# Kernel tuning notes

Measured on AMD Instinct MI355X. Metric: run time of the kernel, lower is better.

Reference implementation:

```python
import jax, jax.numpy as jnp
import numpy as np

B, S, E, H, N = 16384, 256, 128, 128, 34  # batch, state_dim, reduced_lang_dim, mlp hidden, N_task
TEMP = 0.1
EPS = 1e-8  # torch cosine_similarity eps


def setup_inputs() -> dict:
    key = jax.random.key(0)
    ks = jax.random.split(key, 12)
    sc = 0.05
    return {
        "state": jax.random.normal(ks[0], (B, S), dtype=jnp.float32),
        "task_id": jax.random.randint(ks[1], (B,), 0, N),
        "prior": jax.random.normal(ks[2], (B, N), dtype=jnp.float32),
        # stacked weights of the 34 per-task MLPs (Linear(S,H) -> ReLU -> Linear(H,H) -> ReLU -> Linear(H,E))
        "W1": jax.random.normal(ks[3], (N, S, H), dtype=jnp.float32) * sc,
        "b1": jax.random.normal(ks[4], (N, H), dtype=jnp.float32) * sc,
        "W2": jax.random.normal(ks[5], (N, H, H), dtype=jnp.float32) * sc,
        "b2": jax.random.normal(ks[6], (N, H), dtype=jnp.float32) * sc,
        "W3": jax.random.normal(ks[7], (N, H, E), dtype=jnp.float32) * sc,
        "b3": jax.random.normal(ks[8], (N, E), dtype=jnp.float32) * sc,
        "lang_emb": jax.random.normal(ks[9], (N, E), dtype=jnp.float32),
    }


def reference(state, task_id, prior, W1, b1, W2, b2, W3, b3, lang_emb):
    # 34 parallel MLPs as a single batched GEMM stack: [B,S] x [N,S,H] -> [B,N,H]
    h = jax.nn.relu(jnp.einsum('bs,nsh->bnh', state, W1) + b1)
    h = jax.nn.relu(jnp.einsum('bnh,nhk->bnk', h, W2) + b2)
    q = jnp.einsum('bnk,nke->bne', h, W3) + b3            # [B,N,E]
    # normalize (torch.norm division, no eps, then cosine_similarity renormalizes -> unit)
    q = q / jnp.linalg.norm(q, axis=-1, keepdims=True)
    lang = lang_emb[task_id]                              # [B,E]
    lang_n = lang / jnp.maximum(jnp.linalg.norm(lang, axis=-1, keepdims=True), EPS)
    cos_sim = jnp.einsum('bne,be->bn', q, lang_n)         # [B,N]
    log_task_prob = jax.nn.log_softmax(cos_sim / TEMP, axis=-1)
    task_prob_prior = jax.nn.softmax(prior, axis=-1)      # exp(log_softmax(prior))
    latent_vec = jnp.einsum('bne,bn->be', q, task_prob_prior)
    latent_target = jax.lax.stop_gradient(q[jnp.arange(B), task_id])  # detach
    rep_vec = jnp.concatenate([state, latent_vec], axis=-1)           # [B, S+E]
    return rep_vec, log_task_prob, latent_target, latent_vec
```

## Files before the change

kernel.cpp:

```cpp
#include <hip/hip_runtime.h>
#include <hip/hip_bf16.h>
#include <hip/hip_fp16.h>
#include <cstdint>
#include <cstddef>

typedef __bf16 bf16;
typedef __attribute__((ext_vector_type(8))) __bf16 bf16x8;
typedef __attribute__((ext_vector_type(16))) float f32x16;

static_assert(sizeof(bf16x8) == 16, "bf16x8 must be 16B");

#define NTASK 34
#define BTOT 16384
#define WSTRIDE 73728

__device__ __forceinline__ f32x16 mfma32(bf16x8 a, bf16x8 b, f32x16 c) {
  return __builtin_amdgcn_mfma_f32_32x32x16_bf16(a, b, c, 0, 0, 0);
}

__device__ __forceinline__ void gload_lds16(const void* g, void* l) {
  __builtin_amdgcn_global_load_lds((__attribute__((address_space(1))) void*)g,
                                   (__attribute__((address_space(3))) void*)l,
                                   16, 0, 0);
}

__device__ __forceinline__ unsigned pack2(float lo, float hi) {
  union { __bf16 h[2]; unsigned u; } v;
  v.h[0] = (__bf16)lo; v.h[1] = (__bf16)hi;
  return v.u;
}

__device__ __forceinline__ void pl32swap(unsigned &a, unsigned &b) {
  asm volatile("v_permlane32_swap_b32 %0, %1" : "+v"(a), "+v"(b));
}

__global__ void prep_all(const float* __restrict__ W1, const float* __restrict__ W2,
                         const float* __restrict__ W3, const float* __restrict__ b1,
                         const float* __restrict__ b2, const float* __restrict__ b3,
                         const float* __restrict__ state,
                         bf16* __restrict__ wdst, bf16* __restrict__ sdst) {
  int bid = blockIdx.x;
  if (bid < 1190) {
    int idx = bid * 256 + threadIdx.x;
    if (idx >= 304640) return;
    int n = idx / (140 * 64);
    int r = idx - n * (140 * 64);
    int bb = r >> 6, l = r & 63;
    const float *W, *bias; int real, mt, ks, Kt;
    size_t off;
    if (bb < 68)       { W = W1; bias = b1; mt = bb / 17; ks = bb - mt * 17; real = 16; Kt = 256;
                         off = (size_t)bb * 512; }
    else if (bb < 104) { W = W2; bias = b2; int t = bb - 68;  mt = t / 9; ks = t - mt * 9; real = 8; Kt = 128;
                         off = 36864 + (size_t)(bb - 68) * 512; }
    else               { W = W3; bias = b3; int t = bb - 104; mt = t / 9; ks = t - mt * 9; real = 8; Kt = 128;
                         off = 36864 + 18432 + (size_t)(bb - 104) * 512; }
    int col = mt * 32 + (l & 31);
    bf16x8 v;
    if (ks < real) {
      int k0 = ks * 16 + ((l >> 5) << 3);
      const float* s = W + ((size_t)n * Kt + k0) * 128 + col;
#pragma unroll
      for (int j = 0; j < 8; ++j) v[j] = (bf16)s[(size_t)j * 128];
    } else {
#pragma unroll
      for (int j = 0; j < 8; ++j) v[j] = (bf16)0.f;
      if (l < 32) v[0] = (bf16)bias[n * 128 + col];
    }
    *(bf16x8*)(wdst + (size_t)n * WSTRIDE + off + l * 8) = v;
  } else {
    int idx = (bid - 1190) * 256 + threadIdx.x;
    int rb = idx >> 10;
    int r = idx & 1023;
    int ks = r >> 6;
    int l = r & 63;
    int b = rb * 32 + (l & 31);
    int k0 = ks * 16 + ((l >> 5) << 3);
    const float* s = state + (size_t)b * 256 + k0;
    bf16x8 v;
#pragma unroll
    for (int j = 0; j < 8; ++j) v[j] = (bf16)s[j];
    *(bf16x8*)(sdst + (size_t)(rb * 16 + ks) * 512 + l * 8) = v;
  }
}

__global__ void prep_langn(const float* __restrict__ lang, float* __restrict__ out) {
  __shared__ float red[2];
  int n = blockIdx.x;
  int t = threadIdx.x;
  float v = lang[(size_t)n * 128 + t];
  float ss = v * v;
#pragma unroll
  for (int m = 1; m < 64; m <<= 1) ss += __shfl_xor(ss, m);
  if ((t & 63) == 0) red[t >> 6] = ss;
  __syncthreads();
  float s = red[0] + red[1];
  float sc = 1.0f / fmaxf(sqrtf(s), 1e-8f);
  out[(size_t)n * 128 + t] = v * sc;
}

__global__ void prep_pprior(const float* __restrict__ prior, float* __restrict__ ppt) {
  int row = blockIdx.x * 4 + (threadIdx.x >> 6);
  int lane = threadIdx.x & 63;
  float v = (lane < NTASK) ? prior[(size_t)row * NTASK + lane] : -INFINITY;
  float m = v;
#pragma unroll
  for (int mm = 1; mm < 64; mm <<= 1) m = fmaxf(m, __shfl_xor(m, mm));
  float e = (lane < NTASK) ? expf(v - m) : 0.0f;
  float s = e;
#pragma unroll
  for (int mm = 1; mm < 64; mm <<= 1) s += __shfl_xor(s, mm);
  if (lane < NTASK) ppt[(size_t)lane * BTOT + row] = e / s;
}


__global__ void __launch_bounds__(512, 2)
pass1_kernel(const int* __restrict__ task_id, const bf16* __restrict__ wstream,
             const bf16* __restrict__ sf, const float* __restrict__ langn,
             const float* __restrict__ pp_t,
             float* __restrict__ cs_t, __half* __restrict__ lat_part,
             float* __restrict__ out_tgt) {
  __shared__ __align__(16) bf16 shA[36864];
  __shared__ __align__(16) bf16 shB[36864];

  const int tid = threadIdx.x;
  const int l = tid & 63;
  const int w = tid >> 6;
  const int hi = l >> 5;
  const int b = l & 31;
  const int tg = blockIdx.x >> 6;
  const int rg = blockIdx.x & 63;
  const int start = tg * 4 + (tg < 2 ? tg : 2);
  const int cnt = 4 + (tg < 2 ? 1 : 0);
  const int row0 = rg * 256 + w * 32 + b;
  const int rb0 = rg * 8 + w;

  int tidn0 = task_id[row0];

  {
    const bf16* wb0 = wstream + (size_t)start * WSTRIDE;
#pragma unroll
    for (int c = 0; c < 9; ++c)
      gload_lds16(wb0 + c * 4096 + tid * 8, shA + c * 4096 + tid * 8);
  }

  union { unsigned u[4]; bf16x8 v; } cf;
  cf.u[0] = (l < 32) ? 0x3f80u : 0u;
  cf.u[1] = 0u; cf.u[2] = 0u; cf.u[3] = 0u;

  f32x16 z;
#pragma unroll
  for (int i = 0; i < 16; ++i) z[i] = 0.f;
  f32x16 lat[4] = {z, z, z, z};

  const bf16* sb0 = sf + (size_t)rb0 * 8192 + l * 8;

  auto transition = [&](f32x16* acc, bf16x8* f) {
#pragma unroll
    for (int mt = 0; mt < 4; ++mt) {
      unsigned p[8];
#pragma unroll
      for (int q = 0; q < 4; ++q) {
        p[2 * q]     = pack2(fmaxf(acc[mt][4 * q + 0], 0.f), fmaxf(acc[mt][4 * q + 1], 0.f));
        p[2 * q + 1] = pack2(fmaxf(acc[mt][4 * q + 2], 0.f), fmaxf(acc[mt][4 * q + 3], 0.f));
      }
      pl32swap(p[0], p[2]); pl32swap(p[1], p[3]);
      pl32swap(p[4], p[6]); pl32swap(p[5], p[7]);
      union { unsigned u[4]; bf16x8 v; } e, o;
      e.u[0] = p[0]; e.u[1] = p[1]; e.u[2] = p[2]; e.u[3] = p[3];
      o.u[0] = p[4]; o.u[1] = p[5]; o.u[2] = p[6]; o.u[3] = p[7];
      f[2 * mt] = e.v; f[2 * mt + 1] = o.v;
    }
  };

  for (int t = 0; t < cnt; ++t) {
    const int n = start + t;
    const bf16* wbase = wstream + (size_t)n * WSTRIDE;

#pragma unroll
    for (int c = 0; c < 9; ++c)
      gload_lds16(wbase + 36864 + c * 4096 + tid * 8, shB + c * 4096 + tid * 8);

    if (t == 0) {
      asm volatile("s_waitcnt vmcnt(9)" ::: "memory");
      __builtin_amdgcn_s_barrier();
    }

    f32x16 acc[4] = {z, z, z, z};

    bf16x8 s0[4];
#pragma unroll
    for (int i = 0; i < 4; ++i) s0[i] = *(const bf16x8*)(sb0 + i * 512);
#pragma unroll
    for (int ks = 0; ks < 16; ++ks) {
      bf16x8 sv = s0[ks & 3];
      if (ks < 12) s0[ks & 3] = *(const bf16x8*)(sb0 + (ks + 4) * 512);
      __builtin_amdgcn_s_setprio(1);
#pragma unroll
      for (int mt = 0; mt < 4; ++mt) {
        bf16x8 wf = *(const bf16x8*)(shA + ((mt * 17 + ks) << 9) + l * 8);
        acc[mt] = mfma32(wf, sv, acc[mt]);
      }
      __builtin_amdgcn_s_setprio(0);
    }
#pragma unroll
    for (int mt = 0; mt < 4; ++mt) {
      bf16x8 wf = *(const bf16x8*)(shA + ((mt * 17 + 16) << 9) + l * 8);
      acc[mt] = mfma32(wf, cf.v, acc[mt]);
    }

    bf16x8 f2[8];
    transition(acc, f2);

    asm volatile("s_waitcnt vmcnt(0)" ::: "memory");
    __builtin_amdgcn_s_barrier();

    if (t + 1 < cnt) {
      const bf16* wnext = wstream + (size_t)(n + 1) * WSTRIDE;
#pragma unroll
      for (int c = 0; c < 9; ++c)
        gload_lds16(wnext + c * 4096 + tid * 8, shA + c * 4096 + tid * 8);
    }
#pragma unroll
    for (int mt = 0; mt < 4; ++mt) acc[mt] = z;
#pragma unroll
    for (int ks = 0; ks < 8; ++ks) {
      __builtin_amdgcn_s_setprio(1);
#pragma unroll
      for (int mt = 0; mt < 4; ++mt) {
        bf16x8 wf = *(const bf16x8*)(shB + ((mt * 9 + ks) << 9) + l * 8);
        acc[mt] = mfma32(wf, f2[ks], acc[mt]);
      }
      __builtin_amdgcn_s_setprio(0);
    }
#pragma unroll
    for (int mt = 0; mt < 4; ++mt) {
      bf16x8 wf = *(const bf16x8*)(shB + ((mt * 9 + 8) << 9) + l * 8);
      acc[mt] = mfma32(wf, cf.v, acc[mt]);
    }

    bf16x8 f3[8];
    transition(acc, f3);

#pragma unroll
    for (int mt = 0; mt < 4; ++mt) acc[mt] = z;
#pragma unroll
    for (int ks = 0; ks < 8; ++ks) {
      __builtin_amdgcn_s_setprio(1);
#pragma unroll
      for (int mt = 0; mt < 4; ++mt) {
        bf16x8 wf = *(const bf16x8*)(shB + ((36 + mt * 9 + ks) << 9) + l * 8);
        acc[mt] = mfma32(wf, f3[ks], acc[mt]);
      }
      __builtin_amdgcn_s_setprio(0);
    }
#pragma unroll
    for (int mt = 0; mt < 4; ++mt) {
      bf16x8 wf = *(const bf16x8*)(shB + ((36 + mt * 9 + 8) << 9) + l * 8);
      acc[mt] = mfma32(wf, cf.v, acc[mt]);
    }

    float ssq = 0.f, dot = 0.f;
    const float* lgb = langn + (size_t)tidn0 * 128;
#pragma unroll
    for (int mt = 0; mt < 4; ++mt)
#pragma unroll
      for (int q = 0; q < 4; ++q) {
        int c0 = mt * 32 + q * 8 + 4 * hi;
        float4 lg = *(const float4*)(lgb + c0);
        float a0 = acc[mt][4 * q + 0], a1 = acc[mt][4 * q + 1];
        float a2 = acc[mt][4 * q + 2], a3 = acc[mt][4 * q + 3];
        ssq += a0 * a0 + a1 * a1 + a2 * a2 + a3 * a3;
        dot += a0 * lg.x + a1 * lg.y + a2 * lg.z + a3 * lg.w;
      }
    ssq += __shfl_xor(ssq, 32);
    dot += __shfl_xor(dot, 32);
    float inv = rsqrtf(ssq);
    if (l < 32) cs_t[(size_t)row0 * NTASK + n] = dot * inv;
    float pwi = pp_t[(size_t)n * BTOT + row0] * inv;
#pragma unroll
    for (int mt = 0; mt < 4; ++mt) lat[mt] += acc[mt] * pwi;
    if (tidn0 == n) {
#pragma unroll
      for (int mt = 0; mt < 4; ++mt)
#pragma unroll
        for (int q = 0; q < 4; ++q) {
          float4 qv = {acc[mt][4 * q + 0] * inv, acc[mt][4 * q + 1] * inv,
                       acc[mt][4 * q + 2] * inv, acc[mt][4 * q + 3] * inv};
          *(float4*)(out_tgt + (size_t)row0 * 128 + mt * 32 + q * 8 + 4 * hi) = qv;
        }
    }

    asm volatile("s_waitcnt vmcnt(0)" ::: "memory");
    __builtin_amdgcn_s_barrier();
  }

  __half* lp = lat_part + ((size_t)tg * BTOT + row0) * 128;
#pragma unroll
  for (int mt = 0; mt < 4; ++mt)
#pragma unroll
    for (int q = 0; q < 4; ++q) {
      int c0 = mt * 32 + q * 8 + 4 * hi;
      union { __half h[4]; uint2 u; } v;
      v.h[0] = __float2half(lat[mt][4 * q + 0]);
      v.h[1] = __float2half(lat[mt][4 * q + 1]);
      v.h[2] = __float2half(lat[mt][4 * q + 2]);
      v.h[3] = __float2half(lat[mt][4 * q + 3]);
      *(uint2*)(lp + c0) = v.u;
    }
}


__global__ void __launch_bounds__(256)
pass3_kernel(const float* __restrict__ state, const float* __restrict__ cs_t,
             const __half* __restrict__ lat_part,
             float* __restrict__ out_rep, float* __restrict__ out_ltp,
             float* __restrict__ out_lat) {
  int w = threadIdx.x >> 6, l = threadIdx.x & 63;
  size_t row = (size_t)blockIdx.x * 4 + w;

  float c = (l < NTASK) ? cs_t[row * NTASK + l] * 10.0f : -1e30f;
  float cm = c;
#pragma unroll
  for (int mm = 1; mm < 64; mm <<= 1) cm = fmaxf(cm, __shfl_xor(cm, mm));
  float ce = (l < NTASK) ? expf(c - cm) : 0.0f;
  float cs = ce;
#pragma unroll
  for (int mm = 1; mm < 64; mm <<= 1) cs += __shfl_xor(cs, mm);
  if (l < NTASK) out_ltp[row * NTASK + l] = c - cm - logf(cs);

  float2 lv = {0.f, 0.f};
#pragma unroll
  for (int g = 0; g < 8; ++g) {
    __half2 p = *(const __half2*)(lat_part + ((size_t)g * BTOT + row) * 128 + 2 * l);
    lv.x += __low2float(p);
    lv.y += __high2float(p);
  }
  *(float2*)(out_lat + row * 128 + 2 * l) = lv;
  *(float2*)(out_rep + row * 384 + 256 + 2 * l) = lv;

  float4 sv = *(const float4*)(state + row * 256 + l * 4);
  *(float4*)(out_rep + row * 384 + l * 4) = sv;
}


extern "C" void kernel_launch(void* const* d_in, const int* in_sizes, int n_in,
                              void* d_out, int out_size, void* d_ws, size_t ws_size,
                              hipStream_t stream) {
  (void)in_sizes; (void)n_in; (void)out_size; (void)ws_size;
  const float* state = (const float*)d_in[0];
  const int* task_id = (const int*)d_in[1];
  const float* prior = (const float*)d_in[2];
  const float* W1 = (const float*)d_in[3];
  const float* b1 = (const float*)d_in[4];
  const float* W2 = (const float*)d_in[5];
  const float* b2 = (const float*)d_in[6];
  const float* W3 = (const float*)d_in[7];
  const float* b3 = (const float*)d_in[8];
  const float* lang = (const float*)d_in[9];

  char* ws = (char*)d_ws;
  bf16* wstream  = (bf16*)(ws + 0);
  bf16* sf       = (bf16*)(ws + 5013504);
  float* langn   = (float*)(ws + 13402112);
  float* pp_t    = (float*)(ws + 13419520);
  float* cs_t    = (float*)(ws + 15647744);
  __half* lat_part = (__half*)(ws + 17875968);

  float* out = (float*)d_out;
  float* out_rep = out;
  float* out_ltp = out + 6291456;
  float* out_tgt = out + 6848512;
  float* out_lat = out + 8945664;

  prep_all<<<3238, 256, 0, stream>>>(W1, W2, W3, b1, b2, b3, state, wstream, sf);
  prep_langn<<<NTASK, 128, 0, stream>>>(lang, langn);
  prep_pprior<<<4096, 256, 0, stream>>>(prior, pp_t);
  pass1_kernel<<<512, 512, 0, stream>>>(task_id, wstream, sf, langn, pp_t,
                                        cs_t, lat_part, out_tgt);
  pass3_kernel<<<4096, 256, 0, stream>>>(state, cs_t, lat_part,
                                         out_rep, out_ltp, out_lat);
}
```

Baseline: 160.7 us.

## Shrink pass1 blocks to 256 threads with single LDS weight buffer; fuse prior softmax

Pass1 now runs 1024 blocks of 256 threads, each covering 128 rows, and keeps a single 72 KB LDS buffer instead of two. Within each task, the W1 stage, then the W2/W3 stage, are streamed into that buffer in turn, with barriers and partial vmcnt waits so the W3 half can arrive while layer 2 computes. The prior softmax is folded into prep_all as extra blocks, which removes one kernel launch. Less LDS per block may allow more resident blocks, but the weight-load latency is now more exposed because the next load cannot start until compute on the buffer has finished. Each block also handles fewer rows, so weights are fetched from L2 twice as often.

```diff
diff --git a/kernel.cpp b/kernel.cpp
--- a/kernel.cpp
+++ b/kernel.cpp
@@ -37,8 +37,9 @@
 __global__ void prep_all(const float* __restrict__ W1, const float* __restrict__ W2,
                          const float* __restrict__ W3, const float* __restrict__ b1,
                          const float* __restrict__ b2, const float* __restrict__ b3,
-                         const float* __restrict__ state,
-                         bf16* __restrict__ wdst, bf16* __restrict__ sdst) {
+                         const float* __restrict__ state, const float* __restrict__ prior,
+                         bf16* __restrict__ wdst, bf16* __restrict__ sdst,
+                         float* __restrict__ ppt) {
   int bid = blockIdx.x;
   if (bid < 1190) {
     int idx = bid * 256 + threadIdx.x;
@@ -67,7 +68,7 @@
       if (l < 32) v[0] = (bf16)bias[n * 128 + col];
     }
     *(bf16x8*)(wdst + (size_t)n * WSTRIDE + off + l * 8) = v;
-  } else {
+  } else if (bid < 3238) {
     int idx = (bid - 1190) * 256 + threadIdx.x;
     int rb = idx >> 10;
     int r = idx & 1023;
@@ -80,6 +81,18 @@
 #pragma unroll
     for (int j = 0; j < 8; ++j) v[j] = (bf16)s[j];
     *(bf16x8*)(sdst + (size_t)(rb * 16 + ks) * 512 + l * 8) = v;
+  } else {
+    int row = (bid - 3238) * 4 + (threadIdx.x >> 6);
+    int lane = threadIdx.x & 63;
+    float v = (lane < NTASK) ? prior[(size_t)row * NTASK + lane] : -INFINITY;
+    float m = v;
+#pragma unroll
+    for (int mm = 1; mm < 64; mm <<= 1) m = fmaxf(m, __shfl_xor(m, mm));
+    float e = (lane < NTASK) ? expf(v - m) : 0.0f;
+    float s = e;
+#pragma unroll
+    for (int mm = 1; mm < 64; mm <<= 1) s += __shfl_xor(s, mm);
+    if (lane < NTASK) ppt[(size_t)lane * BTOT + row] = e / s;
   }
 }
 
@@ -98,49 +111,34 @@
   out[(size_t)n * 128 + t] = v * sc;
 }
 
-__global__ void prep_pprior(const float* __restrict__ prior, float* __restrict__ ppt) {
-  int row = blockIdx.x * 4 + (threadIdx.x >> 6);
-  int lane = threadIdx.x & 63;
-  float v = (lane < NTASK) ? prior[(size_t)row * NTASK + lane] : -INFINITY;
-  float m = v;
-#pragma unroll
-  for (int mm = 1; mm < 64; mm <<= 1) m = fmaxf(m, __shfl_xor(m, mm));
-  float e = (lane < NTASK) ? expf(v - m) : 0.0f;
-  float s = e;
-#pragma unroll
-  for (int mm = 1; mm < 64; mm <<= 1) s += __shfl_xor(s, mm);
-  if (lane < NTASK) ppt[(size_t)lane * BTOT + row] = e / s;
-}
-
-
-__global__ void __launch_bounds__(512, 2)
+
+__global__ void __launch_bounds__(256, 2)
 pass1_kernel(const int* __restrict__ task_id, const bf16* __restrict__ wstream,
              const bf16* __restrict__ sf, const float* __restrict__ langn,
              const float* __restrict__ pp_t,
              float* __restrict__ cs_t, __half* __restrict__ lat_part,
              float* __restrict__ out_tgt) {
-  __shared__ __align__(16) bf16 shA[36864];
-  __shared__ __align__(16) bf16 shB[36864];
+  __shared__ __align__(16) bf16 shW[36864];
 
   const int tid = threadIdx.x;
   const int l = tid & 63;
   const int w = tid >> 6;
   const int hi = l >> 5;
   const int b = l & 31;
-  const int tg = blockIdx.x >> 6;
-  const int rg = blockIdx.x & 63;
+  const int tg = blockIdx.x >> 7;
+  const int rg = blockIdx.x & 127;
   const int start = tg * 4 + (tg < 2 ? tg : 2);
   const int cnt = 4 + (tg < 2 ? 1 : 0);
-  const int row0 = rg * 256 + w * 32 + b;
-  const int rb0 = rg * 8 + w;
+  const int row0 = rg * 128 + w * 32 + b;
+  const int rb0 = rg * 4 + w;
 
   int tidn0 = task_id[row0];
 
   {
     const bf16* wb0 = wstream + (size_t)start * WSTRIDE;
 #pragma unroll
-    for (int c = 0; c < 9; ++c)
-      gload_lds16(wb0 + c * 4096 + tid * 8, shA + c * 4096 + tid * 8);
+    for (int c = 0; c < 17; ++c)
+      gload_lds16(wb0 + c * 2048 + tid * 8, shW + c * 2048 + tid * 8);
   }
 
   union { unsigned u[4]; bf16x8 v; } cf;
@@ -176,14 +174,8 @@
     const int n = start + t;
     const bf16* wbase = wstream + (size_t)n * WSTRIDE;
 
-#pragma unroll
-    for (int c = 0; c < 9; ++c)
-      gload_lds16(wbase + 36864 + c * 4096 + tid * 8, shB + c * 4096 + tid * 8);
-
-    if (t == 0) {
-      asm volatile("s_waitcnt vmcnt(9)" ::: "memory");
-      __builtin_amdgcn_s_barrier();
-    }
+    asm volatile("s_waitcnt vmcnt(0)" ::: "memory");
+    __builtin_amdgcn_s_barrier();
 
     f32x16 acc[4] = {z, z, z, z};
 
@@ -197,66 +189,78 @@
       __builtin_amdgcn_s_setprio(1);
 #pragma unroll
       for (int mt = 0; mt < 4; ++mt) {
-        bf16x8 wf = *(const bf16x8*)(shA + ((mt * 17 + ks) << 9) + l * 8);
+        bf16x8 wf = *(const bf16x8*)(shW + ((mt * 17 + ks) << 9) + l * 8);
         acc[mt] = mfma32(wf, sv, acc[mt]);
       }
       __builtin_amdgcn_s_setprio(0);
     }
 #pragma unroll
     for (int mt = 0; mt < 4; ++mt) {
-      bf16x8 wf = *(const bf16x8*)(shA + ((mt * 17 + 16) << 9) + l * 8);
+      bf16x8 wf = *(const bf16x8*)(shW + ((mt * 17 + 16) << 9) + l * 8);
       acc[mt] = mfma32(wf, cf.v, acc[mt]);
     }
+
+    __builtin_amdgcn_s_barrier();
+
+#pragma unroll
+    for (int c = 0; c < 18; ++c)
+      gload_lds16(wbase + 36864 + c * 2048 + tid * 8, shW + c * 2048 + tid * 8);
 
     bf16x8 f2[8];
     transition(acc, f2);
 
+    asm volatile("s_waitcnt vmcnt(9)" ::: "memory");
+    __builtin_amdgcn_s_barrier();
+
+#pragma unroll
+    for (int mt = 0; mt < 4; ++mt) acc[mt] = z;
+#pragma unroll
+    for (int ks = 0; ks < 8; ++ks) {
+      __builtin_amdgcn_s_setprio(1);
+#pragma unroll
+      for (int mt = 0; mt < 4; ++mt) {
+        bf16x8 wf = *(const bf16x8*)(shW + ((mt * 9 + ks) << 9) + l * 8);
+        acc[mt] = mfma32(wf, f2[ks], acc[mt]);
+      }
+      __builtin_amdgcn_s_setprio(0);
+    }
+#pragma unroll
+    for (int mt = 0; mt < 4; ++mt) {
+      bf16x8 wf = *(const bf16x8*)(shW + ((mt * 9 + 8) << 9) + l * 8);
+      acc[mt] = mfma32(wf, cf.v, acc[mt]);
+    }
+
+    bf16x8 f3[8];
+    transition(acc, f3);
+
     asm volatile("s_waitcnt vmcnt(0)" ::: "memory");
+    __builtin_amdgcn_s_barrier();
+
+#pragma unroll
+    for (int mt = 0; mt < 4; ++mt) acc[mt] = z;
+#pragma unroll
+    for (int ks = 0; ks < 8; ++ks) {
+      __builtin_amdgcn_s_setprio(1);
+#pragma unroll
+      for (int mt = 0; mt < 4; ++mt) {
+        bf16x8 wf = *(const bf16x8*)(shW + ((36 + mt * 9 + ks) << 9) + l * 8);
+        acc[mt] = mfma32(wf, f3[ks], acc[mt]);
+      }
+      __builtin_amdgcn_s_setprio(0);
+    }
+#pragma unroll
+    for (int mt = 0; mt < 4; ++mt) {
+      bf16x8 wf = *(const bf16x8*)(shW + ((36 + mt * 9 + 8) << 9) + l * 8);
+      acc[mt] = mfma32(wf, cf.v, acc[mt]);
+    }
+
     __builtin_amdgcn_s_barrier();
 
     if (t + 1 < cnt) {
       const bf16* wnext = wstream + (size_t)(n + 1) * WSTRIDE;
 #pragma unroll
-      for (int c = 0; c < 9; ++c)
-        gload_lds16(wnext + c * 4096 + tid * 8, shA + c * 4096 + tid * 8);
-    }
-#pragma unroll
-    for (int mt = 0; mt < 4; ++mt) acc[mt] = z;
-#pragma unroll
-    for (int ks = 0; ks < 8; ++ks) {
-      __builtin_amdgcn_s_setprio(1);
-#pragma unroll
-      for (int mt = 0; mt < 4; ++mt) {
-        bf16x8 wf = *(const bf16x8*)(shB + ((mt * 9 + ks) << 9) + l * 8);
-        acc[mt] = mfma32(wf, f2[ks], acc[mt]);
-      }
-      __builtin_amdgcn_s_setprio(0);
-    }
-#pragma unroll
-    for (int mt = 0; mt < 4; ++mt) {
-      bf16x8 wf = *(const bf16x8*)(shB + ((mt * 9 + 8) << 9) + l * 8);
-      acc[mt] = mfma32(wf, cf.v, acc[mt]);
-    }
-
-    bf16x8 f3[8];
-    transition(acc, f3);
-
-#pragma unroll
-    for (int mt = 0; mt < 4; ++mt) acc[mt] = z;
-#pragma unroll
-    for (int ks = 0; ks < 8; ++ks) {
-      __builtin_amdgcn_s_setprio(1);
-#pragma unroll
-      for (int mt = 0; mt < 4; ++mt) {
-        bf16x8 wf = *(const bf16x8*)(shB + ((36 + mt * 9 + ks) << 9) + l * 8);
-        acc[mt] = mfma32(wf, f3[ks], acc[mt]);
-      }
-      __builtin_amdgcn_s_setprio(0);
-    }
-#pragma unroll
-    for (int mt = 0; mt < 4; ++mt) {
-      bf16x8 wf = *(const bf16x8*)(shB + ((36 + mt * 9 + 8) << 9) + l * 8);
-      acc[mt] = mfma32(wf, cf.v, acc[mt]);
+      for (int c = 0; c < 17; ++c)
+        gload_lds16(wnext + c * 2048 + tid * 8, shW + c * 2048 + tid * 8);
     }
 
     float ssq = 0.f, dot = 0.f;
@@ -289,9 +293,6 @@
           *(float4*)(out_tgt + (size_t)row0 * 128 + mt * 32 + q * 8 + 4 * hi) = qv;
         }
     }
-
-    asm volatile("s_waitcnt vmcnt(0)" ::: "memory");
-    __builtin_amdgcn_s_barrier();
   }
 
   __half* lp = lat_part + ((size_t)tg * BTOT + row0) * 128;
@@ -372,11 +373,11 @@
   float* out_tgt = out + 6848512;
   float* out_lat = out + 8945664;
 
-  prep_all<<<3238, 256, 0, stream>>>(W1, W2, W3, b1, b2, b3, state, wstream, sf);
+  prep_all<<<7334, 256, 0, stream>>>(W1, W2, W3, b1, b2, b3, state, prior,
+                                     wstream, sf, pp_t);
   prep_langn<<<NTASK, 128, 0, stream>>>(lang, langn);
-  prep_pprior<<<4096, 256, 0, stream>>>(prior, pp_t);
-  pass1_kernel<<<512, 512, 0, stream>>>(task_id, wstream, sf, langn, pp_t,
-                                        cs_t, lat_part, out_tgt);
+  pass1_kernel<<<1024, 256, 0, stream>>>(task_id, wstream, sf, langn, pp_t,
+                                         cs_t, lat_part, out_tgt);
   pass3_kernel<<<4096, 256, 0, stream>>>(state, cs_t, lat_part,
                                          out_rep, out_ltp, out_lat);
 }
```

Result: faster. 148.5 us (-7.6%).
